# Performance work log

Hardware: AMD Instinct MI355X
Metric: run time of the kernel (lower is better)

## Reference

```python
import jax, jax.numpy as jnp
import numpy as np

BLOCK = 8  # block_size init kwarg


def _process_block(block):
    """Serial Floyd-Steinberg error diffusion within one (BLOCK, BLOCK) tile."""
    def row_step(next_row_err, row):
        row = row + next_row_err  # add errors diffused from the row above
        def px_step(err_right, px):
            old = px + err_right
            new = jnp.where(old > 127.0, 255.0, 0.0)
            e = old - new
            return e * (7.0 / 16.0), (new, e)
        _, (new_row, errs) = jax.lax.scan(px_step, jnp.zeros((), row.dtype), row)
        z = jnp.zeros((1,), errs.dtype)
        # error at x goes to next row at x-1 (3/16), x (5/16), x+1 (1/16)
        nxt = (5.0 / 16.0) * errs \
            + (3.0 / 16.0) * jnp.concatenate([errs[1:], z]) \
            + (1.0 / 16.0) * jnp.concatenate([z, errs[:-1]])
        return nxt, new_row
    _, out = jax.lax.scan(row_step, jnp.zeros((block.shape[1],), block.dtype), block)
    return out


def _halftone(gray):
    """gray: (N, H, W) float32 in [0,255], H and W multiples of BLOCK."""
    N, H, W = gray.shape
    hb, wb = H // BLOCK, W // BLOCK
    blocks = gray.reshape(N, hb, BLOCK, wb, BLOCK).transpose(0, 1, 3, 2, 4)
    blocks = blocks.reshape(N * hb * wb, BLOCK, BLOCK)
    out = jax.vmap(_process_block)(blocks)
    out = out.reshape(N, hb, wb, BLOCK, BLOCK).transpose(0, 1, 3, 2, 4)
    return out.reshape(N, H, W)


def setup_inputs() -> dict:
    key = jax.random.key(0)
    batch = jax.random.uniform(key, (8, 3, 1024, 1024), dtype=jnp.float32)
    return {"batch": batch}


def reference(batch):
    scaled = batch * 255.0  # (B, 3, H, W)
    # cv2.COLOR_BGR2GRAY coefficients on channels [0,1,2] = [B,G,R]
    gray = 0.114 * scaled[:, 0] + 0.587 * scaled[:, 1] + 0.299 * scaled[:, 2]  # (B,H,W)
    # original swapaxes(0,2) -> halftoning runs on a (W, H) layout
    ht = _halftone(gray.transpose(0, 2, 1)).transpose(0, 2, 1)  # (B,H,W), values 0/255
    out = jnp.broadcast_to(ht[:, None, :, :], scaled.shape)
    out = jnp.where(scaled == 0.0, 0.0, out)  # mask: zero input stays zero
    return out / 255.0
```

## Files before the change

### kernel.cpp

```cpp
#include <hip/hip_runtime.h>


#define IMG_H 1024
#define IMG_W 1024
#define NCH   3

__global__ __launch_bounds__(256, 6)
void fs_halftone_kernel(const float* __restrict__ in, float* __restrict__ out,
                        int n_imgs) {
#pragma clang fp contract(off)
    const int tiles_w = IMG_W / 8;
    const int tiles_per_img = tiles_w * (IMG_H / 8);

    int gtid = blockIdx.x * blockDim.x + threadIdx.x;
    int tile = gtid >> 3;
    int col  = gtid & 7;
    int lane = threadIdx.x & 63;
    int b  = tile / tiles_per_img;
    if (b >= n_imgs) return;
    int t  = tile % tiles_per_img;
    int th = t / tiles_w;
    int tw = t % tiles_w;

    const size_t imgstride = (size_t)IMG_H * IMG_W;
    const size_t col_off   = (size_t)(th * 8) * IMG_W + (size_t)(tw * 8) + (size_t)col;
    const float* base = in  + (size_t)b * NCH * imgstride + col_off;
    float*      obase = out + (size_t)b * NCH * imgstride + col_off;

    float a0[8], a1[8], a2[8];
#pragma unroll
    for (int r = 0; r < 8; ++r) a0[r] = base[0 * imgstride + (size_t)r * IMG_W];
#pragma unroll
    for (int r = 0; r < 8; ++r) a1[r] = base[1 * imgstride + (size_t)r * IMG_W];
#pragma unroll
    for (int r = 0; r < 8; ++r) a2[r] = base[2 * imgstride + (size_t)r * IMG_W];

    float p[8];
    unsigned int zm0 = 0u, zm1 = 0u, zm2 = 0u;
#pragma unroll
    for (int r = 0; r < 8; ++r) {
        float s0 = a0[r] * 255.0f;
        float s1 = a1[r] * 255.0f;
        float s2 = a2[r] * 255.0f;
        if (s0 == 0.0f) zm0 |= 1u << r;
        if (s1 == 0.0f) zm1 |= 1u << r;
        if (s2 == 0.0f) zm2 |= 1u << r;
        p[r] = ((0.114f * s0) + (0.587f * s1)) + (0.299f * s2);
    }

    float nrow[8];
#pragma unroll
    for (int j = 0; j < 8; ++j) nrow[j] = 0.0f;

    unsigned int ob = 0u;

#pragma unroll
    for (int i = 0; i < 8; ++i) {
        float cv[8];
#pragma unroll
        for (int j = 0; j < 8; ++j)
            cv[j] = __shfl(p[j], (lane & ~7) | i);

        float errs[8];
        float er = 0.0f;
        unsigned int onb = 0u;
#pragma unroll
        for (int j = 0; j < 8; ++j) {
            float px  = cv[j] + nrow[j];
            float old = px + er;
            bool  on  = old > 127.0f;
            float nw  = on ? 255.0f : 0.0f;
            float e   = old - nw;
            er = e * 0.4375f;
            errs[j] = e;
            if (on) onb |= 1u << j;
        }
        if (col == i) ob = onb;
#pragma unroll
        for (int j = 0; j < 8; ++j) {
            float en = (j < 7) ? errs[j + 1] : 0.0f;
            float ep = (j > 0) ? errs[j - 1] : 0.0f;
            nrow[j] = ((0.3125f * errs[j]) + (0.1875f * en)) + (0.0625f * ep);
        }
    }

#pragma unroll
    for (int ch = 0; ch < 3; ++ch) {
        unsigned int zm = (ch == 0) ? zm0 : ((ch == 1) ? zm1 : zm2);
#pragma unroll
        for (int r = 0; r < 8; ++r) {
            bool on = (ob >> r) & 1u;
            bool z  = (zm >> r) & 1u;
            obase[ch * imgstride + (size_t)r * IMG_W] = (on && !z) ? 1.0f : 0.0f;
        }
    }
}

extern "C" void kernel_launch(void* const* d_in, const int* in_sizes, int n_in,
                              void* d_out, int out_size, void* d_ws, size_t ws_size,
                              hipStream_t stream) {
    const float* in  = (const float*)d_in[0];
    float*       out = (float*)d_out;

    int n_imgs = in_sizes[0] / (NCH * IMG_H * IMG_W);
    int total_threads = 8 * n_imgs * (IMG_H / 8) * (IMG_W / 8);
    int block = 256;
    int grid = (total_threads + block - 1) / block;
    fs_halftone_kernel<<<grid, block, 0, stream>>>(in, out, n_imgs);
}
```

Before: 38.40 us.

## Split halftone into bit-packed stage and vectorized output write kernel

Stage one computes the halftone and zero masks per 8x8 tile and packs them into 64-bit bitmasks, using shuffle OR reductions, in a workspace buffer. Stage two reads the packed masks and writes the output with 16-byte vector stores per row segment. The aim is better store coalescing than the per-column scalar stores. In exchange it adds a second launch and extra workspace traffic, and it falls back to the fused kernel when the workspace is too small.

Result: slower. 47.88 us (+24.7%).

```diff
diff --git a/kernel.cpp b/kernel.cpp
--- a/kernel.cpp
+++ b/kernel.cpp
@@ -1,13 +1,35 @@
 #include <hip/hip_runtime.h>
+#include <stdint.h>
 
 
 #define IMG_H 1024
 #define IMG_W 1024
 #define NCH   3
 
+typedef float v4f __attribute__((ext_vector_type(4)));
+typedef unsigned long long u64;
+
+__device__ __forceinline__ u64 spread8(unsigned int x) {
+    u64 v = x;
+    v = (v | (v << 28)) & 0x0000000F0000000Full;
+    v = (v | (v << 14)) & 0x0003000300030003ull;
+    v = (v | (v << 7))  & 0x0101010101010101ull;
+    return v;
+}
+
+__device__ __forceinline__ u64 or_reduce8(u64 v) {
+    unsigned int lo = (unsigned int)v, hi = (unsigned int)(v >> 32);
+#pragma unroll
+    for (int d = 1; d < 8; d <<= 1) {
+        lo |= __shfl_xor(lo, d);
+        hi |= __shfl_xor(hi, d);
+    }
+    return ((u64)hi << 32) | lo;
+}
+
 __global__ __launch_bounds__(256, 6)
-void fs_halftone_kernel(const float* __restrict__ in, float* __restrict__ out,
-                        int n_imgs) {
+void fs_stage1(const float* __restrict__ in, unsigned int* __restrict__ rec,
+               int n_imgs) {
 #pragma clang fp contract(off)
     const int tiles_w = IMG_W / 8;
     const int tiles_per_img = tiles_w * (IMG_H / 8);
@@ -23,9 +45,8 @@
     int tw = t % tiles_w;
 
     const size_t imgstride = (size_t)IMG_H * IMG_W;
-    const size_t col_off   = (size_t)(th * 8) * IMG_W + (size_t)(tw * 8) + (size_t)col;
-    const float* base = in  + (size_t)b * NCH * imgstride + col_off;
-    float*      obase = out + (size_t)b * NCH * imgstride + col_off;
+    const float* base = in + (size_t)b * NCH * imgstride
+                      + (size_t)(th * 8) * IMG_W + (size_t)(tw * 8) + (size_t)col;
 
     float a0[8], a1[8], a2[8];
 #pragma unroll
@@ -51,16 +72,13 @@
     float nrow[8];
 #pragma unroll
     for (int j = 0; j < 8; ++j) nrow[j] = 0.0f;
-
     unsigned int ob = 0u;
-
 #pragma unroll
     for (int i = 0; i < 8; ++i) {
         float cv[8];
 #pragma unroll
         for (int j = 0; j < 8; ++j)
             cv[j] = __shfl(p[j], (lane & ~7) | i);
-
         float errs[8];
         float er = 0.0f;
         unsigned int onb = 0u;
@@ -84,6 +102,135 @@
         }
     }
 
+    u64 H  = or_reduce8(spread8(ob)  << col);
+    u64 Z0 = or_reduce8(spread8(zm0) << col);
+    u64 Z1 = or_reduce8(spread8(zm1) << col);
+    u64 Z2 = or_reduce8(spread8(zm2) << col);
+
+    u64 sel = (col < 2) ? H : ((col < 4) ? Z0 : ((col < 6) ? Z1 : Z2));
+    unsigned int w = (col & 1) ? (unsigned int)(sel >> 32) : (unsigned int)sel;
+    rec[gtid] = w;
+}
+
+__global__ __launch_bounds__(256)
+void fs_stage2(const unsigned int* __restrict__ rec, float* __restrict__ out,
+               int n_imgs) {
+    const int tiles_w = IMG_W / 8;
+    const int tiles_per_img = tiles_w * (IMG_H / 8);
+
+    int gtid = blockIdx.x * blockDim.x + threadIdx.x;
+    int tile = gtid >> 1;
+    int hh   = gtid & 1;
+    int b  = tile / tiles_per_img;
+    if (b >= n_imgs) return;
+    int t  = tile % tiles_per_img;
+    int th = t / tiles_w;
+    int tw = t % tiles_w;
+
+    const u64* rp = (const u64*)(rec) + (size_t)tile * 4;
+    u64 H  = rp[0];
+    u64 Z0 = rp[1];
+    u64 Z1 = rp[2];
+    u64 Z2 = rp[3];
+
+    const size_t imgstride = (size_t)IMG_H * IMG_W;
+    float* obase = out + (size_t)b * NCH * imgstride
+                 + (size_t)(th * 8) * IMG_W + (size_t)(tw * 8) + (size_t)(hh * 4);
+
+#pragma unroll
+    for (int ch = 0; ch < 3; ++ch) {
+        u64 Z = (ch == 0) ? Z0 : ((ch == 1) ? Z1 : Z2);
+#pragma unroll
+        for (int r = 0; r < 8; ++r) {
+            v4f v;
+#pragma unroll
+            for (int k = 0; k < 4; ++k) {
+                int bit = r * 8 + hh * 4 + k;
+                bool on = (H >> bit) & 1ull;
+                bool z  = (Z >> bit) & 1ull;
+                v[k] = (on && !z) ? 1.0f : 0.0f;
+            }
+            *(v4f*)(obase + ch * imgstride + (size_t)r * IMG_W) = v;
+        }
+    }
+}
+
+__global__ __launch_bounds__(256, 6)
+void fs_fused(const float* __restrict__ in, float* __restrict__ out,
+              int n_imgs) {
+#pragma clang fp contract(off)
+    const int tiles_w = IMG_W / 8;
+    const int tiles_per_img = tiles_w * (IMG_H / 8);
+
+    int gtid = blockIdx.x * blockDim.x + threadIdx.x;
+    int tile = gtid >> 3;
+    int col  = gtid & 7;
+    int lane = threadIdx.x & 63;
+    int b  = tile / tiles_per_img;
+    if (b >= n_imgs) return;
+    int t  = tile % tiles_per_img;
+    int th = t / tiles_w;
+    int tw = t % tiles_w;
+
+    const size_t imgstride = (size_t)IMG_H * IMG_W;
+    const size_t col_off   = (size_t)(th * 8) * IMG_W + (size_t)(tw * 8) + (size_t)col;
+    const float* base = in  + (size_t)b * NCH * imgstride + col_off;
+    float*      obase = out + (size_t)b * NCH * imgstride + col_off;
+
+    float a0[8], a1[8], a2[8];
+#pragma unroll
+    for (int r = 0; r < 8; ++r) a0[r] = base[0 * imgstride + (size_t)r * IMG_W];
+#pragma unroll
+    for (int r = 0; r < 8; ++r) a1[r] = base[1 * imgstride + (size_t)r * IMG_W];
+#pragma unroll
+    for (int r = 0; r < 8; ++r) a2[r] = base[2 * imgstride + (size_t)r * IMG_W];
+
+    float p[8];
+    unsigned int zm0 = 0u, zm1 = 0u, zm2 = 0u;
+#pragma unroll
+    for (int r = 0; r < 8; ++r) {
+        float s0 = a0[r] * 255.0f;
+        float s1 = a1[r] * 255.0f;
+        float s2 = a2[r] * 255.0f;
+        if (s0 == 0.0f) zm0 |= 1u << r;
+        if (s1 == 0.0f) zm1 |= 1u << r;
+        if (s2 == 0.0f) zm2 |= 1u << r;
+        p[r] = ((0.114f * s0) + (0.587f * s1)) + (0.299f * s2);
+    }
+
+    float nrow[8];
+#pragma unroll
+    for (int j = 0; j < 8; ++j) nrow[j] = 0.0f;
+    unsigned int ob = 0u;
+#pragma unroll
+    for (int i = 0; i < 8; ++i) {
+        float cv[8];
+#pragma unroll
+        for (int j = 0; j < 8; ++j)
+            cv[j] = __shfl(p[j], (lane & ~7) | i);
+        float errs[8];
+        float er = 0.0f;
+        unsigned int onb = 0u;
+#pragma unroll
+        for (int j = 0; j < 8; ++j) {
+            float px  = cv[j] + nrow[j];
+            float old = px + er;
+            bool  on  = old > 127.0f;
+            float nw  = on ? 255.0f : 0.0f;
+            float e   = old - nw;
+            er = e * 0.4375f;
+            errs[j] = e;
+            if (on) onb |= 1u << j;
+        }
+        if (col == i) ob = onb;
+#pragma unroll
+        for (int j = 0; j < 8; ++j) {
+            float en = (j < 7) ? errs[j + 1] : 0.0f;
+            float ep = (j > 0) ? errs[j - 1] : 0.0f;
+            nrow[j] = ((0.3125f * errs[j]) + (0.1875f * en)) + (0.0625f * ep);
+        }
+    }
+
 #pragma unroll
     for (int ch = 0; ch < 3; ++ch) {
         unsigned int zm = (ch == 0) ? zm0 : ((ch == 1) ? zm1 : zm2);
@@ -103,8 +250,17 @@
     float*       out = (float*)d_out;
 
     int n_imgs = in_sizes[0] / (NCH * IMG_H * IMG_W);
-    int total_threads = 8 * n_imgs * (IMG_H / 8) * (IMG_W / 8);
-    int block = 256;
-    int grid = (total_threads + block - 1) / block;
-    fs_halftone_kernel<<<grid, block, 0, stream>>>(in, out, n_imgs);
-}
+    int total_tiles = n_imgs * (IMG_H / 8) * (IMG_W / 8);
+    size_t rec_bytes = (size_t)total_tiles * 32;
+
+    if (ws_size >= rec_bytes) {
+        unsigned int* rec = (unsigned int*)d_ws;
+        int thr1 = 8 * total_tiles;
+        fs_stage1<<<(thr1 + 255) / 256, 256, 0, stream>>>(in, rec, n_imgs);
+        int thr2 = 2 * total_tiles;
+        fs_stage2<<<(thr2 + 255) / 256, 256, 0, stream>>>(rec, out, n_imgs);
+    } else {
+        int thr = 8 * total_tiles;
+        fs_fused<<<(thr + 255) / 256, 256, 0, stream>>>(in, out, n_imgs);
+    }
+}
```
